# Optimization experiments

Hardware: AMD Instinct MI355X
Metric: run time of the kernel (lower is better)

Reference implementation:

```python
import jax, jax.numpy as jnp
import numpy as np

DIM = 512
HEADS = 8
WIN = 64            # sqrt(num_patches) = sqrt(4096)
NUM_PATCHES = WIN * WIN
B = 8
N = 1024
NUM_REL = (2 * WIN - 1) ** 2 + 3


def _relative_position_index():
    # Same construction as RelativePositionBias.__init__ (torch meshgrid default is 'ij')
    coords = np.stack(np.meshgrid(np.arange(WIN), np.arange(WIN), indexing='ij'))  # [2,W,W]
    cf = coords.reshape(2, -1)                              # [2, W*W]
    rel = cf[:, :, None] - cf[:, None, :]                   # [2, P, P]
    rel = rel.transpose(1, 2, 0).copy()                     # [P, P, 2]
    rel[:, :, 0] += WIN - 1
    rel[:, :, 1] += WIN - 1
    rel[:, :, 0] *= 2 * WIN - 1
    return rel.sum(-1).astype(np.int32)                     # [P, P]


def setup_inputs() -> dict:
    key = jax.random.key(0)
    k_x, k_ids, k_qkv, k_proj, k_tab = jax.random.split(key, 5)
    x = jax.random.normal(k_x, (B, N, DIM), dtype=jnp.float32)
    ids_keep = jax.random.randint(k_ids, (B, N), 0, NUM_PATCHES, dtype=jnp.int32)
    w_qkv = jax.random.normal(k_qkv, (DIM, 3 * DIM), dtype=jnp.float32) * 0.02
    w_proj = jax.random.normal(k_proj, (DIM, DIM), dtype=jnp.float32) * 0.02
    b_proj = jnp.zeros((DIM,), dtype=jnp.float32)
    rel_table = jax.random.normal(k_tab, (NUM_REL, HEADS), dtype=jnp.float32) * 0.02
    rel_index = jnp.asarray(_relative_position_index())
    return {"x": x, "ids_keep": ids_keep, "w_qkv": w_qkv, "w_proj": w_proj,
            "b_proj": b_proj, "rel_table": rel_table, "rel_index": rel_index}


def reference(x, ids_keep, w_qkv, w_proj, b_proj, rel_table, rel_index):
    Bb, Nn, C = x.shape
    H = rel_table.shape[1]
    D = C // H
    # QKV projection (no bias, matching qkv_bias=False)
    qkv = (x @ w_qkv).reshape(Bb, Nn, 3, H, D).transpose(2, 0, 3, 1, 4)  # [3,B,H,N,D]
    q, k, v = qkv[0], qkv[1], qkv[2]
    # Masked relative position bias: double gather via index lookup, then table lookup.
    # Equivalent to gathering rows/cols of the full [P,P] bias with ids_keep.
    idx = rel_index[ids_keep[:, :, None], ids_keep[:, None, :]]          # [B,N,N]
    bias = rel_table[idx].transpose(0, 3, 1, 2)                          # [B,H,N,N]
    # Scaled dot-product attention with additive bias (xformers applies 1/sqrt(D))
    scale = 1.0 / jnp.sqrt(jnp.asarray(D, dtype=x.dtype))
    scores = jnp.einsum('bhnd,bhmd->bhnm', q, k) * scale + bias
    attn = jax.nn.softmax(scores, axis=-1)
    out = jnp.einsum('bhnm,bhmd->bnhd', attn, v).reshape(Bb, Nn, C)
    return out @ w_proj + b_proj
```

## Files before the change

### kernel.cpp

```cpp
#include <hip/hip_runtime.h>

typedef __attribute__((ext_vector_type(8))) __bf16 bf16x8;
typedef __attribute__((ext_vector_type(4))) float f32x4;
typedef __attribute__((ext_vector_type(16))) float f32x16;
typedef __attribute__((ext_vector_type(4))) unsigned int u32x4;
typedef unsigned short u16;
typedef unsigned int u32;

__device__ __forceinline__ u16 f2bf(float f) {
  __bf16 h = (__bf16)f;
  return *(u16*)&h;
}
__device__ __forceinline__ float bf2f(u16 h) {
  return __uint_as_float(((u32)h) << 16);
}
__device__ __forceinline__ u32 pack2(float lo, float hi) {
  return (u32)f2bf(lo) | ((u32)f2bf(hi) << 16);
}
__device__ __forceinline__ f32x4 mfma16(bf16x8 a, bf16x8 b, f32x4 c) {
  return __builtin_amdgcn_mfma_f32_16x16x32_bf16(a, b, c, 0, 0, 0);
}
__device__ __forceinline__ f32x16 mfma32(bf16x8 a, bf16x8 b, f32x16 c) {
  return __builtin_amdgcn_mfma_f32_32x32x16_bf16(a, b, c, 0, 0, 0);
}
__device__ __forceinline__ void gl16(const void* g, void* l) {
  __builtin_amdgcn_global_load_lds(
      (const __attribute__((address_space(1))) void*)g,
      (__attribute__((address_space(3))) void*)l, 16, 0, 0);
}

__global__ void cvt_to_bf16(const float* __restrict__ src, u16* __restrict__ dst, int n) {
  const int i = (blockIdx.x * 256 + threadIdx.x) * 4;
  if (i + 3 < n) {
    const float4 v = *(const float4*)(src + i);
    ushort4 o; o.x = f2bf(v.x); o.y = f2bf(v.y); o.z = f2bf(v.z); o.w = f2bf(v.w);
    *(ushort4*)(dst + i) = o;
  }
}

__global__ __launch_bounds__(256) void prep_misc(
    const float* __restrict__ w_qkv, const float* __restrict__ w_proj,
    const float* __restrict__ rel_tab,
    u16* __restrict__ wT, u16* __restrict__ wpT, u16* __restrict__ tabb)
{
  __shared__ float tile[32][33];
  const int b = blockIdx.x;
  const int tid = threadIdx.x;
  if (b < 1024) {
    const float* src; u16* dst; int C, c0, r0;
    if (b < 768) { src = w_qkv; dst = wT; C = 1536; c0 = (b % 48) * 32; r0 = (b / 48) * 32; }
    else { const int bb = b - 768; src = w_proj; dst = wpT; C = 512; c0 = (bb % 16) * 32; r0 = (bb / 16) * 32; }
    const int tx = tid & 31, ty = tid >> 5;
    for (int i = ty; i < 32; i += 8)
      tile[i][tx] = src[(size_t)(r0 + i) * C + c0 + tx];
    __syncthreads();
    for (int i = ty; i < 32; i += 8)
      dst[(size_t)(c0 + i) * 512 + r0 + tx] = f2bf(tile[tx][i]);
  } else {
    const int i = ((b - 1024) * 256 + tid) * 4;
    if (i + 3 < 16131 * 8) {
      const float4 v = *(const float4*)(rel_tab + i);
      ushort4 o; o.x = f2bf(v.x); o.y = f2bf(v.y); o.z = f2bf(v.z); o.w = f2bf(v.w);
      *(ushort4*)(tabb + i) = o;
    }
  }
}

template<int MODE>
__global__ __launch_bounds__(256, 2) void gemm_bt(
    const u16* __restrict__ A, const u16* __restrict__ Bt,
    u16* __restrict__ out0, u16* __restrict__ out1,
    float* __restrict__ fout, const float* __restrict__ bias)
{
  __shared__ u16 As[128][32];
  __shared__ u16 Bs[128][32];
  const int tid = threadIdx.x;
  const int w = tid >> 6, l = tid & 63;
  const int lr = l & 15, lg = l >> 4;
  const int wr = w >> 1, wc = w & 1;
  const int m0 = blockIdx.y * 128, n0 = blockIdx.x * 128;
  const int sl = (lr >> 1) & 3;
  const int cA = lg ^ sl;

  f32x4 acc[4][4] = {};

  for (int k0 = 0; k0 < 512; k0 += 32) {
#pragma unroll
    for (int it = 0; it < 2; ++it) {
      const int ch = it * 256 + tid;
      const int row = ch >> 2, cslot = ch & 3;
      const int csrc = cslot ^ ((row >> 1) & 3);
      gl16(A  + (size_t)(m0 + row) * 512 + k0 + csrc * 8, (u16*)As + ch * 8);
      gl16(Bt + (size_t)(n0 + row) * 512 + k0 + csrc * 8, (u16*)Bs + ch * 8);
    }
    __syncthreads();
    bf16x8 af[4], bfr[4];
#pragma unroll
    for (int mi = 0; mi < 4; ++mi)
      af[mi] = *(const bf16x8*)&As[wr * 64 + mi * 16 + lr][cA * 8];
#pragma unroll
    for (int nj = 0; nj < 4; ++nj)
      bfr[nj] = *(const bf16x8*)&Bs[wc * 64 + nj * 16 + lr][cA * 8];
#pragma unroll
    for (int mi = 0; mi < 4; ++mi)
#pragma unroll
      for (int nj = 0; nj < 4; ++nj)
        acc[mi][nj] = mfma16(af[mi], bfr[nj], acc[mi][nj]);
    __syncthreads();
  }

#pragma unroll
  for (int mi = 0; mi < 4; ++mi)
#pragma unroll
    for (int nj = 0; nj < 4; ++nj) {
      const int i0 = m0 + wr * 64 + mi * 16 + lg * 4;
      const int j  = n0 + wc * 64 + nj * 16 + lr;
      if (MODE == 0) {
        const int bb = j >> 10, n = j & 1023;
        const bool isQ = i0 < 512;
        const int f = isQ ? i0 : i0 - 512;
        const int h = f >> 6, d0 = f & 63;
        const float scl = isQ ? 0.125f : 1.0f;
        u16* dst = isQ ? out0 : out1;
        const size_t off = ((size_t)(bb * 8 + h) << 16) +
            ((((n >> 5) * 4 + (d0 >> 4)) * 2 + ((d0 >> 3) & 1)) << 8) +
            ((n & 31) << 3) + (d0 & 7);
        ushort4 o;
        o.x = f2bf(acc[mi][nj][0] * scl); o.y = f2bf(acc[mi][nj][1] * scl);
        o.z = f2bf(acc[mi][nj][2] * scl); o.w = f2bf(acc[mi][nj][3] * scl);
        *(ushort4*)(dst + off) = o;
      } else if (MODE == 1) {
        const int bb = i0 >> 10, m = i0 & 1023;
        const int h = j >> 6, d = j & 63;
        const size_t off = ((size_t)(bb * 8 + h) << 16) +
            ((((m >> 6) * 4 + ((m >> 4) & 3)) * 2 + ((m >> 2) & 1)) << 9) +
            (d << 3) + (((m >> 3) & 1) << 2);
        ushort4 o;
        o.x = f2bf(acc[mi][nj][0]); o.y = f2bf(acc[mi][nj][1]);
        o.z = f2bf(acc[mi][nj][2]); o.w = f2bf(acc[mi][nj][3]);
        *(ushort4*)(out0 + off) = o;
      } else {
        const float4 bp = *(const float4*)(bias + i0);
        float4 o;
        o.x = acc[mi][nj][0] + bp.x; o.y = acc[mi][nj][1] + bp.y;
        o.z = acc[mi][nj][2] + bp.z; o.w = acc[mi][nj][3] + bp.w;
        *(float4*)(fout + (size_t)j * 512 + i0) = o;
      }
    }
}

__global__ __launch_bounds__(1024) void flash_attn(
    const u16* __restrict__ Qs, const u16* __restrict__ Ks,
    const u16* __restrict__ Vs, const int* __restrict__ ids_keep,
    const u16* __restrict__ tab_bf,
    u16* __restrict__ attn_out)
{
  __shared__ union {
    u16 tabL[16129 * 4];
    float comb[8][33][64];
  } sm;
  __shared__ int bofs[1024];

  const int bid = blockIdx.x;
  const int bb = bid & 7;
  const int r2 = bid >> 3;
  const int hp = r2 & 1;
  const int g64 = r2 >> 1;
  const int tid = threadIdx.x;
  const int wv = tid >> 6;
  const int hloc = wv & 3;
  const int qs = (wv >> 2) & 1;
  const int kvh = wv >> 3;
  const int l = tid & 63, l31 = l & 31, hi5 = l >> 5;
  const int h = hp * 4 + hloc;
  const int t0 = kvh * 8;

  for (int e = tid; e < 16129; e += 1024)
    *(ushort4*)&sm.tabL[e * 4] = *(const ushort4*)(tab_bf + (size_t)e * 8 + hp * 4);
  {
    const int id = ids_keep[bb * 1024 + tid];
    bofs[tid] = (8064 - ((id >> 6) * 127 + (id & 63))) * 8;
  }

  const int nloc = g64 * 64 + qs * 32 + l31;
  const int idn = ids_keep[bb * 1024 + nloc];
  const int base = ((idn >> 6) * 127 + (idn & 63)) * 8 + hloc * 2;

  const size_t hb = (size_t)(bb * 8 + h) << 16;
  const int g32 = g64 * 2 + qs;

  f32x16 acc0 = {}, acc1 = {};
  float lsum = 0.f;

  bf16x8 qf[4];
#pragma unroll
  for (int dch = 0; dch < 4; ++dch)
    qf[dch] = *(const bf16x8*)(Qs + hb + (size_t)(((g32 * 4 + dch) * 2 + hi5) * 256 + l31 * 8));

  __syncthreads();

  const char* tb = (const char*)sm.tabL;

  for (int t = t0; t < t0 + 8; ++t) {
    u32 pk[2][4][2];
#pragma unroll
    for (int u = 0; u < 2; ++u) {
      bf16x8 kc[4];
#pragma unroll
      for (int dch = 0; dch < 4; ++dch)
        kc[dch] = *(const bf16x8*)(Ks + hb +
            (size_t)((((2 * t + u) * 4 + dch) * 2 + hi5) * 256 + l31 * 8));
      f32x16 s = {};
      s = mfma32(kc[0], qf[0], s);
      s = mfma32(kc[1], qf[1], s);
      s = mfma32(kc[2], qf[2], s);
      s = mfma32(kc[3], qf[3], s);
#pragma unroll
      for (int a = 0; a < 4; ++a) {
        const int4 bo = *(const int4*)&bofs[t * 64 + u * 32 + a * 8 + hi5 * 4];
        const float b0 = bf2f(*(const u16*)(tb + base + bo.x));
        const float b1 = bf2f(*(const u16*)(tb + base + bo.y));
        const float b2 = bf2f(*(const u16*)(tb + base + bo.z));
        const float b3 = bf2f(*(const u16*)(tb + base + bo.w));
        float p0 = __expf(s[a * 4 + 0] + b0);
        float p1 = __expf(s[a * 4 + 1] + b1);
        float p2 = __expf(s[a * 4 + 2] + b2);
        float p3 = __expf(s[a * 4 + 3] + b3);
        lsum += (p0 + p1) + (p2 + p3);
        pk[u][a][0] = pack2(p0, p1);
        pk[u][a][1] = pack2(p2, p3);
      }
    }

#pragma unroll
    for (int cp = 0; cp < 4; ++cp) {
      bf16x8 vc[2];
#pragma unroll
      for (int dc = 0; dc < 2; ++dc)
        vc[dc] = *(const bf16x8*)(Vs + hb +
            (size_t)(((t * 4 + cp) * 2 + hi5) * 512 + (dc * 32 + l31) * 8));
      const int u = cp >> 1, cc = cp & 1;
      union { u32x4 u4; bf16x8 v; } pb;
      pb.u4 = (u32x4){pk[u][2 * cc][0], pk[u][2 * cc][1],
                      pk[u][2 * cc + 1][0], pk[u][2 * cc + 1][1]};
      acc0 = mfma32(vc[0], pb.v, acc0);
      acc1 = mfma32(vc[1], pb.v, acc1);
    }
  }

  lsum += __shfl_xor(lsum, 32);

  __syncthreads();
  const int slot = wv & 7;
  if (kvh == 1) {
#pragma unroll
    for (int r = 0; r < 16; ++r) sm.comb[slot][r][l]      = acc0[r];
#pragma unroll
    for (int r = 0; r < 16; ++r) sm.comb[slot][16 + r][l] = acc1[r];
    sm.comb[slot][32][l] = lsum;
  }
  __syncthreads();
  if (kvh == 0) {
    const float inv = 1.0f / (lsum + sm.comb[slot][32][l]);
    const int nglob = bb * 1024 + nloc;
#pragma unroll
    for (int dc = 0; dc < 2; ++dc) {
      const f32x16& av = dc ? acc1 : acc0;
#pragma unroll
      for (int rq = 0; rq < 4; ++rq) {
        const int d = dc * 32 + rq * 8 + hi5 * 4;
        ushort4 o;
        o.x = f2bf((av[rq * 4 + 0] + sm.comb[slot][dc * 16 + rq * 4 + 0][l]) * inv);
        o.y = f2bf((av[rq * 4 + 1] + sm.comb[slot][dc * 16 + rq * 4 + 1][l]) * inv);
        o.z = f2bf((av[rq * 4 + 2] + sm.comb[slot][dc * 16 + rq * 4 + 2][l]) * inv);
        o.w = f2bf((av[rq * 4 + 3] + sm.comb[slot][dc * 16 + rq * 4 + 3][l]) * inv);
        *(ushort4*)(attn_out + (size_t)nglob * 512 + h * 64 + d) = o;
      }
    }
  }
}

extern "C" void kernel_launch(void* const* d_in, const int* in_sizes, int n_in,
                              void* d_out, int out_size, void* d_ws, size_t ws_size,
                              hipStream_t stream) {
  const float* x        = (const float*)d_in[0];
  const int*   ids      = (const int*)d_in[1];
  const float* w_qkv    = (const float*)d_in[2];
  const float* w_proj   = (const float*)d_in[3];
  const float* b_proj   = (const float*)d_in[4];
  const float* rel_tab  = (const float*)d_in[5];
  float* out = (float*)d_out;

  char* ws = (char*)d_ws;
  u16* xb   = (u16*)(ws);
  u16* wT   = (u16*)(ws + 8388608);
  u16* wpT  = (u16*)(ws + 9961472);
  u16* Qsw  = (u16*)(ws + 10485760);
  u16* Ksw  = (u16*)(ws + 18874368);
  u16* Vsw  = (u16*)(ws + 27262976);
  u16* tabb = (u16*)(ws + 35651584);
  u16* attn = xb;

  cvt_to_bf16<<<4096, 256, 0, stream>>>(x, xb, 8 * 1024 * 512);
  prep_misc<<<1151, 256, 0, stream>>>(w_qkv, w_proj, rel_tab, wT, wpT, tabb);

  gemm_bt<0><<<dim3(64, 8), 256, 0, stream>>>(wT, xb, Qsw, Ksw, nullptr, nullptr);
  gemm_bt<1><<<dim3(4, 64), 256, 0, stream>>>(xb, wT + 1024 * 512, Vsw, nullptr, nullptr, nullptr);

  flash_attn<<<dim3(256), 1024, 0, stream>>>(Qsw, Ksw, Vsw, ids, tabb, attn);

  gemm_bt<2><<<dim3(64, 4), 256, 0, stream>>>(wpT, attn, nullptr, nullptr, out, b_proj);
}
```

Baseline: 94.50 us.

## Merge prep kernels, fuse QK and V projections, split bias table per head pair

Merges the x conversion and weight/table prep into one launch, and merges the QK and V projection GEMMs into one 768-block launch, cutting the number of launches from six to four. In the attention kernel, the shared-memory bias table is split into two planes of two heads each, so every wave reads 4-byte pairs from its own plane instead of from an interleaved 8-byte record. This changes bank-access patterns and offset arithmetic. Removing the bounds check in the x conversion relies on the exact input size.

```diff
diff --git a/kernel.cpp b/kernel.cpp
--- a/kernel.cpp
+++ b/kernel.cpp
@@ -29,27 +29,27 @@
       (__attribute__((address_space(3))) void*)l, 16, 0, 0);
 }
 
-__global__ void cvt_to_bf16(const float* __restrict__ src, u16* __restrict__ dst, int n) {
-  const int i = (blockIdx.x * 256 + threadIdx.x) * 4;
-  if (i + 3 < n) {
-    const float4 v = *(const float4*)(src + i);
-    ushort4 o; o.x = f2bf(v.x); o.y = f2bf(v.y); o.z = f2bf(v.z); o.w = f2bf(v.w);
-    *(ushort4*)(dst + i) = o;
-  }
-}
-
-__global__ __launch_bounds__(256) void prep_misc(
-    const float* __restrict__ w_qkv, const float* __restrict__ w_proj,
-    const float* __restrict__ rel_tab,
-    u16* __restrict__ wT, u16* __restrict__ wpT, u16* __restrict__ tabb)
+__global__ __launch_bounds__(256) void prep_all(
+    const float* __restrict__ x, const float* __restrict__ w_qkv,
+    const float* __restrict__ w_proj, const float* __restrict__ rel_tab,
+    u16* __restrict__ xb, u16* __restrict__ wT, u16* __restrict__ wpT,
+    u16* __restrict__ tabb)
 {
   __shared__ float tile[32][33];
   const int b = blockIdx.x;
   const int tid = threadIdx.x;
-  if (b < 1024) {
+  if (b < 4096) {
+    const int i = (b * 256 + tid) * 4;
+    const float4 v = *(const float4*)(x + i);
+    ushort4 o; o.x = f2bf(v.x); o.y = f2bf(v.y); o.z = f2bf(v.z); o.w = f2bf(v.w);
+    *(ushort4*)(xb + i) = o;
+    return;
+  }
+  const int bp = b - 4096;
+  if (bp < 1024) {
     const float* src; u16* dst; int C, c0, r0;
-    if (b < 768) { src = w_qkv; dst = wT; C = 1536; c0 = (b % 48) * 32; r0 = (b / 48) * 32; }
-    else { const int bb = b - 768; src = w_proj; dst = wpT; C = 512; c0 = (bb % 16) * 32; r0 = (bb / 16) * 32; }
+    if (bp < 768) { src = w_qkv; dst = wT; C = 1536; c0 = (bp % 48) * 32; r0 = (bp / 48) * 32; }
+    else { const int bb = bp - 768; src = w_proj; dst = wpT; C = 512; c0 = (bb % 16) * 32; r0 = (bb / 16) * 32; }
     const int tx = tid & 31, ty = tid >> 5;
     for (int i = ty; i < 32; i += 8)
       tile[i][tx] = src[(size_t)(r0 + i) * C + c0 + tx];
@@ -57,7 +57,7 @@
     for (int i = ty; i < 32; i += 8)
       dst[(size_t)(c0 + i) * 512 + r0 + tx] = f2bf(tile[tx][i]);
   } else {
-    const int i = ((b - 1024) * 256 + tid) * 4;
+    const int i = ((bp - 1024) * 256 + tid) * 4;
     if (i + 3 < 16131 * 8) {
       const float4 v = *(const float4*)(rel_tab + i);
       ushort4 o; o.x = f2bf(v.x); o.y = f2bf(v.y); o.z = f2bf(v.z); o.w = f2bf(v.w);
@@ -66,10 +66,93 @@
   }
 }
 
-template<int MODE>
-__global__ __launch_bounds__(256, 2) void gemm_bt(
+__global__ __launch_bounds__(256, 2) void gemm_qkv(
+    const u16* __restrict__ xb, const u16* __restrict__ wT,
+    u16* __restrict__ Qs, u16* __restrict__ Ks, u16* __restrict__ Vs)
+{
+  __shared__ u16 As[128][32];
+  __shared__ u16 Bs[128][32];
+  const int bid = blockIdx.x;
+  const bool modeV = bid >= 512;
+  const u16* A; const u16* Bt; int m0, n0;
+  if (!modeV) {
+    A = wT; Bt = xb;
+    m0 = (bid >> 6) * 128; n0 = (bid & 63) * 128;
+  } else {
+    const int r = bid - 512;
+    A = xb; Bt = wT + 1024 * 512;
+    m0 = (r & 63) * 128; n0 = (r >> 6) * 128;
+  }
+  const int tid = threadIdx.x;
+  const int w = tid >> 6, l = tid & 63;
+  const int lr = l & 15, lg = l >> 4;
+  const int wr = w >> 1, wc = w & 1;
+  const int sl = (lr >> 1) & 3;
+  const int cA = lg ^ sl;
+
+  f32x4 acc[4][4] = {};
+
+  for (int k0 = 0; k0 < 512; k0 += 32) {
+#pragma unroll
+    for (int it = 0; it < 2; ++it) {
+      const int ch = it * 256 + tid;
+      const int row = ch >> 2, cslot = ch & 3;
+      const int csrc = cslot ^ ((row >> 1) & 3);
+      gl16(A  + (size_t)(m0 + row) * 512 + k0 + csrc * 8, (u16*)As + ch * 8);
+      gl16(Bt + (size_t)(n0 + row) * 512 + k0 + csrc * 8, (u16*)Bs + ch * 8);
+    }
+    __syncthreads();
+    bf16x8 af[4], bfr[4];
+#pragma unroll
+    for (int mi = 0; mi < 4; ++mi)
+      af[mi] = *(const bf16x8*)&As[wr * 64 + mi * 16 + lr][cA * 8];
+#pragma unroll
+    for (int nj = 0; nj < 4; ++nj)
+      bfr[nj] = *(const bf16x8*)&Bs[wc * 64 + nj * 16 + lr][cA * 8];
+#pragma unroll
+    for (int mi = 0; mi < 4; ++mi)
+#pragma unroll
+      for (int nj = 0; nj < 4; ++nj)
+        acc[mi][nj] = mfma16(af[mi], bfr[nj], acc[mi][nj]);
+    __syncthreads();
+  }
+
+#pragma unroll
+  for (int mi = 0; mi < 4; ++mi)
+#pragma unroll
+    for (int nj = 0; nj < 4; ++nj) {
+      const int i0 = m0 + wr * 64 + mi * 16 + lg * 4;
+      const int j  = n0 + wc * 64 + nj * 16 + lr;
+      if (!modeV) {
+        const int bb = j >> 10, n = j & 1023;
+        const bool isQ = i0 < 512;
+        const int f = isQ ? i0 : i0 - 512;
+        const int h = f >> 6, d0 = f & 63;
+        const float scl = isQ ? 0.125f : 1.0f;
+        u16* dst = isQ ? Qs : Ks;
+        const size_t off = ((size_t)(bb * 8 + h) << 16) +
+            ((((n >> 5) * 4 + (d0 >> 4)) * 2 + ((d0 >> 3) & 1)) << 8) +
+            ((n & 31) << 3) + (d0 & 7);
+        ushort4 o;
+        o.x = f2bf(acc[mi][nj][0] * scl); o.y = f2bf(acc[mi][nj][1] * scl);
+        o.z = f2bf(acc[mi][nj][2] * scl); o.w = f2bf(acc[mi][nj][3] * scl);
+        *(ushort4*)(dst + off) = o;
+      } else {
+        const int bb = i0 >> 10, m = i0 & 1023;
+        const int h = j >> 6, d = j & 63;
+        const size_t off = ((size_t)(bb * 8 + h) << 16) +
+            ((((m >> 6) * 4 + ((m >> 4) & 3)) * 2 + ((m >> 2) & 1)) << 9) +
+            (d << 3) + (((m >> 3) & 1) << 2);
+        ushort4 o;
+        o.x = f2bf(acc[mi][nj][0]); o.y = f2bf(acc[mi][nj][1]);
+        o.z = f2bf(acc[mi][nj][2]); o.w = f2bf(acc[mi][nj][3]);
+        *(ushort4*)(Vs + off) = o;
+      }
+    }
+}
+
+__global__ __launch_bounds__(256, 2) void gemm_proj(
     const u16* __restrict__ A, const u16* __restrict__ Bt,
-    u16* __restrict__ out0, u16* __restrict__ out1,
     float* __restrict__ fout, const float* __restrict__ bias)
 {
   __shared__ u16 As[128][32];
@@ -115,37 +198,11 @@
     for (int nj = 0; nj < 4; ++nj) {
       const int i0 = m0 + wr * 64 + mi * 16 + lg * 4;
       const int j  = n0 + wc * 64 + nj * 16 + lr;
-      if (MODE == 0) {
-        const int bb = j >> 10, n = j & 1023;
-        const bool isQ = i0 < 512;
-        const int f = isQ ? i0 : i0 - 512;
-        const int h = f >> 6, d0 = f & 63;
-        const float scl = isQ ? 0.125f : 1.0f;
-        u16* dst = isQ ? out0 : out1;
-        const size_t off = ((size_t)(bb * 8 + h) << 16) +
-            ((((n >> 5) * 4 + (d0 >> 4)) * 2 + ((d0 >> 3) & 1)) << 8) +
-            ((n & 31) << 3) + (d0 & 7);
-        ushort4 o;
-        o.x = f2bf(acc[mi][nj][0] * scl); o.y = f2bf(acc[mi][nj][1] * scl);
-        o.z = f2bf(acc[mi][nj][2] * scl); o.w = f2bf(acc[mi][nj][3] * scl);
-        *(ushort4*)(dst + off) = o;
-      } else if (MODE == 1) {
-        const int bb = i0 >> 10, m = i0 & 1023;
-        const int h = j >> 6, d = j & 63;
-        const size_t off = ((size_t)(bb * 8 + h) << 16) +
-            ((((m >> 6) * 4 + ((m >> 4) & 3)) * 2 + ((m >> 2) & 1)) << 9) +
-            (d << 3) + (((m >> 3) & 1) << 2);
-        ushort4 o;
-        o.x = f2bf(acc[mi][nj][0]); o.y = f2bf(acc[mi][nj][1]);
-        o.z = f2bf(acc[mi][nj][2]); o.w = f2bf(acc[mi][nj][3]);
-        *(ushort4*)(out0 + off) = o;
-      } else {
-        const float4 bp = *(const float4*)(bias + i0);
-        float4 o;
-        o.x = acc[mi][nj][0] + bp.x; o.y = acc[mi][nj][1] + bp.y;
-        o.z = acc[mi][nj][2] + bp.z; o.w = acc[mi][nj][3] + bp.w;
-        *(float4*)(fout + (size_t)j * 512 + i0) = o;
-      }
+      const float4 bp = *(const float4*)(bias + i0);
+      float4 o;
+      o.x = acc[mi][nj][0] + bp.x; o.y = acc[mi][nj][1] + bp.y;
+      o.z = acc[mi][nj][2] + bp.z; o.w = acc[mi][nj][3] + bp.w;
+      *(float4*)(fout + (size_t)j * 512 + i0) = o;
     }
 }
 
@@ -156,7 +213,7 @@
     u16* __restrict__ attn_out)
 {
   __shared__ union {
-    u16 tabL[16129 * 4];
+    u16 tabL[2][16129 * 2];
     float comb[8][33][64];
   } sm;
   __shared__ int bofs[1024];
@@ -175,16 +232,20 @@
   const int h = hp * 4 + hloc;
   const int t0 = kvh * 8;
 
-  for (int e = tid; e < 16129; e += 1024)
-    *(ushort4*)&sm.tabL[e * 4] = *(const ushort4*)(tab_bf + (size_t)e * 8 + hp * 4);
+  for (int e = tid; e < 16129 * 2; e += 1024) {
+    const int hi = e >= 16129;
+    const int ee = hi ? e - 16129 : e;
+    *(u32*)&sm.tabL[hi][ee * 2] =
+        *(const u32*)(tab_bf + (size_t)ee * 8 + hp * 4 + hi * 2);
+  }
   {
     const int id = ids_keep[bb * 1024 + tid];
-    bofs[tid] = (8064 - ((id >> 6) * 127 + (id & 63))) * 8;
+    bofs[tid] = (8064 - ((id >> 6) * 127 + (id & 63))) * 4;
   }
 
   const int nloc = g64 * 64 + qs * 32 + l31;
   const int idn = ids_keep[bb * 1024 + nloc];
-  const int base = ((idn >> 6) * 127 + (idn & 63)) * 8 + hloc * 2;
+  const int base = ((idn >> 6) * 127 + (idn & 63)) * 4 + (hloc & 1) * 2;
 
   const size_t hb = (size_t)(bb * 8 + h) << 16;
   const int g32 = g64 * 2 + qs;
@@ -199,7 +260,7 @@
 
   __syncthreads();
 
-  const char* tb = (const char*)sm.tabL;
+  const char* tb = (const char*)sm.tabL[hloc >> 1];
 
   for (int t = t0; t < t0 + 8; ++t) {
     u32 pk[2][4][2];
@@ -301,13 +362,8 @@
   u16* tabb = (u16*)(ws + 35651584);
   u16* attn = xb;
 
-  cvt_to_bf16<<<4096, 256, 0, stream>>>(x, xb, 8 * 1024 * 512);
-  prep_misc<<<1151, 256, 0, stream>>>(w_qkv, w_proj, rel_tab, wT, wpT, tabb);
-
-  gemm_bt<0><<<dim3(64, 8), 256, 0, stream>>>(wT, xb, Qsw, Ksw, nullptr, nullptr);
-  gemm_bt<1><<<dim3(4, 64), 256, 0, stream>>>(xb, wT + 1024 * 512, Vsw, nullptr, nullptr, nullptr);
-
+  prep_all<<<5247, 256, 0, stream>>>(x, w_qkv, w_proj, rel_tab, xb, wT, wpT, tabb);
+  gemm_qkv<<<768, 256, 0, stream>>>(xb, wT, Qsw, Ksw, Vsw);
   flash_attn<<<dim3(256), 1024, 0, stream>>>(Qsw, Ksw, Vsw, ids, tabb, attn);
-
-  gemm_bt<2><<<dim3(64, 4), 256, 0, stream>>>(wpT, attn, nullptr, nullptr, out, b_proj);
-}
+  gemm_proj<<<dim3(64, 4), 256, 0, stream>>>(wpT, attn, out, b_proj);
+}
```

Measured after the change: 91.17 us. 3.5% less time.
